# Performance work log

Hardware: AMD Instinct MI355X
Metric: run time of the kernel (lower is better)

## Reference

```python
import jax, jax.numpy as jnp
import numpy as np

N, D, R, L, E, EP = 50000, 256, 16, 2, 300000, 100000
SCALING = 16.0 / 16.0  # alpha / rank


def _ln(x, g, b, eps=1e-5):
    mu = x.mean(-1, keepdims=True)
    var = ((x - mu) ** 2).mean(-1, keepdims=True)
    return (x - mu) * jax.lax.rsqrt(var + eps) * g + b


def setup_inputs() -> dict:
    key = jax.random.key(0)
    ks = iter(jax.random.split(key, 32))
    f = lambda shp, s=0.05: jax.random.normal(next(ks), shp, jnp.float32) * s
    return dict(
        x=f((2, N, D), 1.0),
        W_in=f((2, D, D)), b_in=f((2, D)),
        lora_A=f((2, R, D)), lora_B=f((2, D, R), 0.01),
        pn_g=jnp.ones((2, D), jnp.float32), pn_b=jnp.zeros((2, D), jnp.float32),
        W_self=f((L, 2, D, D)), W_neigh=f((L, 2, D, D)), b_sage=f((L, 2, D)),
        ln_g=jnp.ones((L, 2, D), jnp.float32), ln_b=jnp.zeros((L, 2, D), jnp.float32),
        Wv=f((2, D, D)), bv=f((2, D)), Wo=f((2, D, D)), bo=f((2, D)),
        e_src=jax.random.randint(next(ks), (2, E), 0, N, jnp.int32),
        e_dst=jax.random.randint(next(ks), (2, E), 0, N, jnp.int32),
        pos_src=jax.random.randint(next(ks), (EP,), 0, N, jnp.int32),
        pos_dst=jax.random.randint(next(ks), (EP,), 0, N, jnp.int32),
        neg_src=jax.random.randint(next(ks), (EP,), 0, N, jnp.int32),
        neg_dst=jax.random.randint(next(ks), (EP,), 0, N, jnp.int32),
    )


def reference(x, W_in, b_in, lora_A, lora_B, pn_g, pn_b, W_self, W_neigh,
              b_sage, ln_g, ln_b, Wv, bv, Wo, bo,
              e_src, e_dst, pos_src, pos_dst, neg_src, neg_dst):
    # ---- per-type input projection + LoRA adapter + patient LayerNorm ----
    base = jnp.einsum('tnd,tod->tno', x, W_in) + b_in[:, None]
    ad = jnp.einsum('tnr,tdr->tnd', jnp.einsum('tnd,trd->tnr', x, lora_A), lora_B) * SCALING
    h = _ln(base + ad, pn_g[:, None], pn_b[:, None])  # [2, N, D]

    def seg_mean(v, i):  # mean aggregation over incoming edges
        s = jax.ops.segment_sum(v, i, num_segments=N)
        c = jax.ops.segment_sum(jnp.ones((i.shape[0], 1), v.dtype), i, num_segments=N)
        return s / jnp.maximum(c, 1.0)

    # ---- SAGE layers over blocks (relation 0: a->b, relation 1: b->a) ----
    for i in range(L):
        msgs = jax.vmap(lambda hr, sr: hr[sr])(h, e_src)      # [2, E, D], src type r
        agg = jax.vmap(seg_mean)(msgs, e_dst)                 # agg[r] lands at dst type 1-r
        neigh = agg[::-1]                                     # neigh[t] for node type t
        h_new = (jnp.einsum('tnd,tod->tno', h, W_self[i])
                 + jnp.einsum('tnd,tod->tno', neigh, W_neigh[i])
                 + b_sage[i][:, None])
        if i == L - 1:
            # nn.MultiheadAttention with seq_len=1: softmax over 1 key == 1,
            # so attn_out = out_proj(v_proj(x)).
            v = jnp.einsum('tnd,tod->tno', h_new, Wv) + bv[:, None]
            h_new = jnp.einsum('tnd,tod->tno', v, Wo) + bo[:, None]
        if i > 0:
            h_new = h_new + h  # residual (shapes always match)
        h = _ln(h_new, ln_g[i][:, None], ln_b[i][:, None])
        # dropout is identity at inference

    # ---- dot-product edge predictor on pos/neg graphs for etype (a, rel, b) ----
    h_a, h_b = h[0], h[1]
    pos_score = jnp.sum(h_a[pos_src] * h_b[pos_dst], axis=-1)
    neg_score = jnp.sum(h_a[neg_src] * h_b[neg_dst], axis=-1)
    return pos_score, neg_score
```

## Files before the change

### kernel.cpp

```cpp
#include <hip/hip_runtime.h>

#define D 256
#define BM 128
#define BN 128
#define BK 64
#define SCAN_NB 64
#define SCAN_T (SCAN_NB * 256)

typedef __attribute__((ext_vector_type(8))) short bf16x8;
typedef __attribute__((ext_vector_type(4))) float f32x4;
typedef __attribute__((ext_vector_type(4))) unsigned int u32x4;

union frag_cvt { u32x4 u; bf16x8 h; };

__device__ __forceinline__ unsigned short bf16_rn(float f) {
    const unsigned int u = __float_as_uint(f);
    return (unsigned short)((u + 0x7FFFu + ((u >> 16) & 1u)) >> 16);
}
__device__ __forceinline__ float bf16_to_f32(unsigned short s) {
    return __uint_as_float(((unsigned int)s) << 16);
}
__device__ __forceinline__ int xcd_logical(int bx, int NB) {
    const int q = NB >> 3, rem = NB & 7;
    const int xcd = bx & 7, slot = bx >> 3;
    return (xcd < rem) ? xcd * (q + 1) + slot
                       : rem * (q + 1) + (xcd - rem) * q + slot;
}

__global__ __launch_bounds__(256) void pre1_kernel(
    const float* __restrict__ W_in, const float* __restrict__ lA, const float* __restrict__ lB,
    unsigned short* __restrict__ win_eff,
    const float* __restrict__ W_self, unsigned short* __restrict__ ws0,
    const float* __restrict__ W_neigh, unsigned short* __restrict__ wn0,
    const float* __restrict__ Wo, const float* __restrict__ Wv, float* __restrict__ wvo,
    const float* __restrict__ bvp, const float* __restrict__ bo, float* __restrict__ bvo)
{
    const int b = blockIdx.x, tid = threadIdx.x;
    if (b < 512) {
        const int t = b >> 8, o = b & 255;
        float acc = W_in[((size_t)t * D + o) * D + tid];
        const float* Br = lB + ((size_t)t * D + o) * 16;
        const float* At = lA + (size_t)t * 16 * D;
        #pragma unroll
        for (int r = 0; r < 16; ++r) acc = fmaf(Br[r], At[r * D + tid], acc);
        win_eff[((size_t)t * D + o) * D + tid] = bf16_rn(acc);
    } else if (b < 1024) {
        const int i = (b - 512) * 256 + tid;
        ws0[i] = bf16_rn(W_self[i]);
    } else if (b < 1536) {
        const int i = (b - 1024) * 256 + tid;
        wn0[i] = bf16_rn(W_neigh[i]);
    } else if (b < 2048) {
        const int t = (b - 1536) >> 8, p = (b - 1536) & 255;
        const float* Xr = Wo + ((size_t)t * D + p) * D;
        const float* Yt = Wv + (size_t)t * D * D;
        float acc = 0.f;
        for (int o = 0; o < D; ++o) acc = fmaf(Xr[o], Yt[(size_t)o * D + tid], acc);
        wvo[((size_t)t * D + p) * D + tid] = acc;
    } else {
        const int t = b - 2048;
        const float* Mr = Wo + ((size_t)t * D + tid) * D;
        const float* vr = bvp + (size_t)t * D;
        float acc = bo[(size_t)t * D + tid];
        for (int o = 0; o < D; ++o) acc = fmaf(Mr[o], vr[o], acc);
        bvo[(size_t)t * D + tid] = acc;
    }
}

__global__ __launch_bounds__(256) void pre2_kernel(
    const float* __restrict__ wvo,
    const float* __restrict__ W_self1, unsigned short* __restrict__ ws1,
    const float* __restrict__ W_neigh1, unsigned short* __restrict__ wn1,
    const float* __restrict__ b_sage1, const float* __restrict__ bvo, float* __restrict__ b1e)
{
    const int b = blockIdx.x, tid = threadIdx.x;
    if (b < 512) {
        const int t = b >> 8, p = b & 255;
        const float* Xr = wvo + ((size_t)t * D + p) * D;
        const float* Yt = W_self1 + (size_t)t * D * D;
        float acc = 0.f;
        for (int o = 0; o < D; ++o) acc = fmaf(Xr[o], Yt[(size_t)o * D + tid], acc);
        ws1[((size_t)t * D + p) * D + tid] = bf16_rn(acc);
    } else if (b < 1024) {
        const int t = (b - 512) >> 8, p = (b - 512) & 255;
        const float* Xr = wvo + ((size_t)t * D + p) * D;
        const float* Yt = W_neigh1 + (size_t)t * D * D;
        float acc = 0.f;
        for (int o = 0; o < D; ++o) acc = fmaf(Xr[o], Yt[(size_t)o * D + tid], acc);
        wn1[((size_t)t * D + p) * D + tid] = bf16_rn(acc);
    } else {
        const int t = b - 1024;
        const float* Mr = wvo + ((size_t)t * D + tid) * D;
        const float* vr = b_sage1 + (size_t)t * D;
        float acc = bvo[(size_t)t * D + tid];
        for (int o = 0; o < D; ++o) acc = fmaf(Mr[o], vr[o], acc);
        b1e[(size_t)t * D + tid] = acc;
    }
}

__device__ __forceinline__ void load_bfrag(const unsigned short* __restrict__ Wp,
                                           int n0, int wn, int cidx, int rgrp,
                                           int kh, bf16x8 (&bq)[4][4])
{
    #pragma unroll
    for (int n = 0; n < 4; ++n) {
        const int o = n0 + wn + n * 16 + cidx;
        #pragma unroll
        for (int kk = 0; kk < 4; ++kk) {
            frag_cvt c;
            c.u = *(const u32x4*)(Wp + (size_t)o * D + kh * 128 + kk * 32 + rgrp * 8);
            bq[n][kk] = c.h;
        }
    }
}

__device__ __forceinline__ void gload_tile(const unsigned short* __restrict__ Abase,
                                           int r0, int kt, int tid, char* lbuf)
{
    const int wbase = (tid >> 6) << 10;
    #pragma unroll
    for (int c = 0; c < 4; ++c) {
        const int p   = c * 4096 + tid * 16;
        const int row = p >> 7;
        const int lwb = p & 127;
        const int lg  = lwb ^ ((row & 7) << 4);
        const unsigned short* g = Abase + (size_t)(r0 + row) * D + kt + (lg >> 1);
        char* l = lbuf + c * 4096 + wbase;
        __builtin_amdgcn_global_load_lds(
            (const __attribute__((address_space(1))) unsigned int*)g,
            (__attribute__((address_space(3))) unsigned int*)l, 16, 0, 0);
    }
}

__global__ __launch_bounds__(256, 2) void gemm_bf16_kernel(
    const unsigned short* __restrict__ A, const unsigned short* __restrict__ W1,
    const unsigned short* __restrict__ A2, const unsigned short* __restrict__ W2,
    const float* __restrict__ bias,
    unsigned short* __restrict__ Cbf, int M, int swap2)
{
    const int t   = blockIdx.z;
    const int logical = xcd_logical(blockIdx.x, gridDim.x);
    const int m0  = (logical >> 1) * BM;
    const int n0  = (logical & 1) * BN;
    const int tid = threadIdx.x;
    const int lane = tid & 63;
    const int wid  = tid >> 6;
    const int wm = (wid >> 1) * 64;
    const int wn = (wid & 1) * 64;
    const int rgrp = lane >> 4;
    const int cidx = lane & 15;

    __shared__ __align__(16) unsigned short SH[16384];
    char* AsB0 = (char*)SH;
    char* AsB1 = (char*)SH + 16384;

    const int t2 = swap2 ? (1 - t) : t;
    const unsigned short* Aps[2] = { A  + (size_t)t  * M * D, A2 + (size_t)t2 * M * D };
    const unsigned short* Wps[2] = { W1 + (size_t)t  * D * D, W2 + (size_t)t  * D * D };

    f32x4 acc[4][4];
    #pragma unroll
    for (int i = 0; i < 4; ++i)
        #pragma unroll
        for (int j = 0; j < 4; ++j)
            acc[i][j] = (f32x4){0.f, 0.f, 0.f, 0.f};

    bf16x8 bq[2][4][4];
    gload_tile(Aps[0], m0, 0, tid, AsB0);
    load_bfrag(Wps[0], n0, wn, cidx, rgrp, 0, bq[0]);

    #pragma unroll
    for (int idx = 0; idx < 8; ++idx) {
        __syncthreads();
        if (idx < 7)
            gload_tile(Aps[(idx + 1) >> 2], m0, ((idx + 1) & 3) * BK, tid,
                       (idx & 1) ? AsB0 : AsB1);
        if ((idx & 1) == 1 && idx < 7) {
            const int nh = (idx >> 1) + 1;
            load_bfrag(Wps[nh >> 1], n0, wn, cidx, rgrp, nh & 1, bq[nh & 1]);
        }
        const char* cb = (idx & 1) ? AsB1 : AsB0;
        const int half = idx >> 1;
        #pragma unroll
        for (int ks = 0; ks < 2; ++ks) {
            const int kb = ks * 64 + rgrp * 16;
            bf16x8 af[4];
            #pragma unroll
            for (int m = 0; m < 4; ++m) {
                const int row = wm + m * 16 + cidx;
                const int sw  = (row * 128 + kb) ^ ((row & 7) << 4);
                frag_cvt c; c.u = *(const u32x4*)(cb + sw); af[m] = c.h;
            }
            #pragma unroll
            for (int m = 0; m < 4; ++m)
                #pragma unroll
                for (int n = 0; n < 4; ++n)
                    acc[m][n] = __builtin_amdgcn_mfma_f32_16x16x32_bf16(
                        af[m], bq[half & 1][n][(idx & 1) * 2 + ks], acc[m][n], 0, 0, 0);
        }
        __syncthreads();
    }

    unsigned short* Ct = Cbf + (size_t)t * M * D;
    #pragma unroll
    for (int h = 0; h < 2; ++h) {
        __syncthreads();
        if ((wid >> 1) == h) {
            #pragma unroll
            for (int n = 0; n < 4; ++n) {
                const int col = wn + n * 16 + cidx;
                const float bc = bias[t * D + n0 + col];
                #pragma unroll
                for (int m = 0; m < 4; ++m) {
                    const int rw = (wm & 63) + m * 16 + rgrp * 4;
                    #pragma unroll
                    for (int i = 0; i < 4; ++i)
                        SH[(rw + i) * 136 + col] = bf16_rn(acc[m][n][i] + bc);
                }
            }
        }
        __syncthreads();
        #pragma unroll
        for (int it = 0; it < 2; ++it) {
            const int g   = tid + it * 256;
            const int row = g >> 3;
            const int cg  = g & 7;
            const int grow = m0 + h * 64 + row;
            if (grow < M) {
                const u32x4 lo = *(const u32x4*)&SH[row * 136 + cg * 16];
                const u32x4 hi = *(const u32x4*)&SH[row * 136 + cg * 16 + 8];
                u32x4* dst = (u32x4*)(Ct + (size_t)grow * D + n0 + cg * 16);
                dst[0] = lo;
                dst[1] = hi;
            }
        }
    }
}

__global__ __launch_bounds__(128, 2) void gemm_in_kernel(
    const float* __restrict__ X, const unsigned short* __restrict__ Wb,
    const float* __restrict__ bias, unsigned short* __restrict__ Cbf, int M)
{
    const int t   = blockIdx.z;
    const int logical = xcd_logical(blockIdx.x, gridDim.x);
    const int m0  = (logical >> 1) * 64;
    const int n0  = (logical & 1) * BN;
    const int tid = threadIdx.x;
    const int lane = tid & 63;
    const int wid  = tid >> 6;
    const int wn = wid * 64;
    const int rgrp = lane >> 4;
    const int cidx = lane & 15;

    __shared__ __align__(16) unsigned short SH[8704];
    char* AsB = (char*)SH;

    const float* Xp = X + (size_t)t * M * D;
    const unsigned short* Wp = Wb + (size_t)t * D * D;

    f32x4 acc[4][4];
    #pragma unroll
    for (int i = 0; i < 4; ++i)
        #pragma unroll
        for (int j = 0; j < 4; ++j)
            acc[i][j] = (f32x4){0.f, 0.f, 0.f, 0.f};

    bf16x8 bq[2][4][4];
    float4 xr0[4], xr1[4];
    #pragma unroll
    for (int it = 0; it < 4; ++it) {
        const int g = tid + it * 128;
        const int row = g >> 3;
        const int kg = g & 7;
        const int ar = min(m0 + row, M - 1);
        xr0[it] = *(const float4*)(Xp + (size_t)ar * D + kg * 8);
        xr1[it] = *(const float4*)(Xp + (size_t)ar * D + kg * 8 + 4);
    }
    load_bfrag(Wp, n0, wn, cidx, rgrp, 0, bq[0]);

    #pragma unroll
    for (int kt_i = 0; kt_i < 4; ++kt_i) {
        #pragma unroll
        for (int it = 0; it < 4; ++it) {
            const int g = tid + it * 128;
            const int row = g >> 3;
            const int kg = g & 7;
            unsigned int w[4];
            w[0] = ((unsigned int)bf16_rn(xr0[it].y) << 16) | bf16_rn(xr0[it].x);
            w[1] = ((unsigned int)bf16_rn(xr0[it].w) << 16) | bf16_rn(xr0[it].z);
            w[2] = ((unsigned int)bf16_rn(xr1[it].y) << 16) | bf16_rn(xr1[it].x);
            w[3] = ((unsigned int)bf16_rn(xr1[it].w) << 16) | bf16_rn(xr1[it].z);
            const int sw = ((row * BK + kg * 8) * 2) ^ ((row & 7) << 4);
            *(u32x4*)(AsB + sw) = (u32x4){w[0], w[1], w[2], w[3]};
        }
        __syncthreads();
        if (kt_i < 3) {
            const int kt = (kt_i + 1) * BK;
            #pragma unroll
            for (int it = 0; it < 4; ++it) {
                const int g = tid + it * 128;
                const int row = g >> 3;
                const int kg = g & 7;
                const int ar = min(m0 + row, M - 1);
                xr0[it] = *(const float4*)(Xp + (size_t)ar * D + kt + kg * 8);
                xr1[it] = *(const float4*)(Xp + (size_t)ar * D + kt + kg * 8 + 4);
            }
        }
        if (kt_i == 1) load_bfrag(Wp, n0, wn, cidx, rgrp, 1, bq[1]);
        #pragma unroll
        for (int ks = 0; ks < 2; ++ks) {
            const int kb = ks * 64 + rgrp * 16;
            bf16x8 af[4];
            #pragma unroll
            for (int m = 0; m < 4; ++m) {
                const int row = m * 16 + cidx;
                const int sw  = (row * 128 + kb) ^ ((row & 7) << 4);
                frag_cvt c; c.u = *(u32x4*)(AsB + sw); af[m] = c.h;
            }
            #pragma unroll
            for (int m = 0; m < 4; ++m)
                #pragma unroll
                for (int n = 0; n < 4; ++n)
                    acc[m][n] = __builtin_amdgcn_mfma_f32_16x16x32_bf16(
                        af[m], bq[kt_i >> 1][n][(kt_i & 1) * 2 + ks], acc[m][n], 0, 0, 0);
        }
        __syncthreads();
    }

    #pragma unroll
    for (int n = 0; n < 4; ++n) {
        const int col = wn + n * 16 + cidx;
        const float bc = bias[t * D + n0 + col];
        #pragma unroll
        for (int m = 0; m < 4; ++m) {
            const int rowb = m * 16 + rgrp * 4;
            #pragma unroll
            for (int i = 0; i < 4; ++i)
                SH[(rowb + i) * 136 + col] = bf16_rn(acc[m][n][i] + bc);
        }
    }
    __syncthreads();
    unsigned short* Ct = Cbf + (size_t)t * M * D;
    #pragma unroll
    for (int it = 0; it < 4; ++it) {
        const int g   = tid + it * 128;
        const int row = g >> 3;
        const int cg  = g & 7;
        const int grow = m0 + row;
        if (grow < M) {
            const u32x4 lo = *(const u32x4*)&SH[row * 136 + cg * 16];
            const u32x4 hi = *(const u32x4*)&SH[row * 136 + cg * 16 + 8];
            u32x4* dst = (u32x4*)(Ct + (size_t)grow * D + n0 + cg * 16);
            dst[0] = lo;
            dst[1] = hi;
        }
    }
}

__global__ __launch_bounds__(256) void ln_wave_kernel(
    const unsigned short* __restrict__ in_bf, const unsigned short* __restrict__ res_bf,
    const float* __restrict__ g, const float* __restrict__ b,
    unsigned short* __restrict__ out_bf, int N)
{
    const int row  = (blockIdx.x * 256 + threadIdx.x) >> 6;
    const int lane = threadIdx.x & 63;
    if (row >= 2 * N) return;
    const int t = (row >= N) ? 1 : 0;
    const ushort4 iv = *(const ushort4*)(in_bf + (size_t)row * D + lane * 4);
    float4 v = make_float4(bf16_to_f32(iv.x), bf16_to_f32(iv.y),
                           bf16_to_f32(iv.z), bf16_to_f32(iv.w));
    if (res_bf) {
        const ushort4 rv = *(const ushort4*)(res_bf + (size_t)row * D + lane * 4);
        v.x += bf16_to_f32(rv.x); v.y += bf16_to_f32(rv.y);
        v.z += bf16_to_f32(rv.z); v.w += bf16_to_f32(rv.w);
    }
    float s = v.x + v.y + v.z + v.w;
    #pragma unroll
    for (int off = 32; off > 0; off >>= 1) s += __shfl_xor(s, off);
    const float mu = s * (1.0f / 256.0f);
    const float4 dl = make_float4(v.x - mu, v.y - mu, v.z - mu, v.w - mu);
    float q = dl.x * dl.x + dl.y * dl.y + dl.z * dl.z + dl.w * dl.w;
    #pragma unroll
    for (int off = 32; off > 0; off >>= 1) q += __shfl_xor(q, off);
    const float rstd = rsqrtf(q * (1.0f / 256.0f) + 1e-5f);
    const float4 gv = *(const float4*)(g + (size_t)t * D + lane * 4);
    const float4 bv = *(const float4*)(b + (size_t)t * D + lane * 4);
    ushort4 ob;
    ob.x = bf16_rn(dl.x * rstd * gv.x + bv.x);
    ob.y = bf16_rn(dl.y * rstd * gv.y + bv.y);
    ob.z = bf16_rn(dl.z * rstd * gv.z + bv.z);
    ob.w = bf16_rn(dl.w * rstd * gv.w + bv.w);
    *(ushort4*)(out_bf + (size_t)row * D + lane * 4) = ob;
}

__global__ void count_kernel(const int* __restrict__ e_dst, int* __restrict__ cnt,
                             int E2, int N, int E)
{
    const int i = blockIdx.x * 256 + threadIdx.x;
    if (i >= E2) return;
    const int t = i / E;
    atomicAdd(&cnt[(size_t)t * N + e_dst[i]], 1);
}

__global__ __launch_bounds__(256) void scan1_kernel(const int* __restrict__ cnt,
                                                    int* __restrict__ texcl,
                                                    int* __restrict__ bsum, int n, int c)
{
    __shared__ int ts[256];
    const int tid = threadIdx.x;
    const int gt  = blockIdx.x * 256 + tid;
    const int b   = gt * c;
    const int e   = min(b + c, n);
    int s = 0;
    for (int i = b; i < e; ++i) s += cnt[i];
    ts[tid] = s;
    __syncthreads();
    #pragma unroll
    for (int off = 1; off < 256; off <<= 1) {
        const int v = (tid >= off) ? ts[tid - off] : 0;
        __syncthreads();
        ts[tid] += v;
        __syncthreads();
    }
    texcl[gt] = ts[tid] - s;
    if (tid == 255) bsum[blockIdx.x] = ts[255];
}

__global__ __launch_bounds__(64) void scan2_kernel(int* __restrict__ bsum,
                                                   int* __restrict__ bbase,
                                                   int* __restrict__ offs, int n, int nb)
{
    const int lane = threadIdx.x;
    int v = (lane < nb) ? bsum[lane] : 0;
    int s = v;
    #pragma unroll
    for (int off = 1; off < 64; off <<= 1) {
        const int u = __shfl_up(s, off);
        if (lane >= off) s += u;
    }
    if (lane < nb) bbase[lane] = s - v;
    if (lane == 63) offs[n] = s;
}

__global__ __launch_bounds__(256) void scan3_kernel(const int* __restrict__ cnt,
                                                    const int* __restrict__ texcl,
                                                    const int* __restrict__ bbase,
                                                    int* __restrict__ offs, int n, int c)
{
    const int tid = threadIdx.x;
    const int gt  = blockIdx.x * 256 + tid;
    const int b   = gt * c;
    const int e   = min(b + c, n);
    int base = bbase[blockIdx.x] + texcl[gt];
    for (int i = b; i < e; ++i) { offs[i] = base; base += cnt[i]; }
}

__global__ void fill_kernel(const int* __restrict__ e_src, const int* __restrict__ e_dst,
                            const int* __restrict__ offs, int* __restrict__ cur,
                            int* __restrict__ sorted, int E2, int N, int E)
{
    const int i = blockIdx.x * 256 + threadIdx.x;
    if (i >= E2) return;
    const int t = i / E;
    const int idx = t * N + e_dst[i];
    const int pos = offs[idx] + atomicAdd(&cur[idx], 1);
    sorted[pos] = e_src[i];
}

__global__ __launch_bounds__(256) void agg_kernel(
    const unsigned short* __restrict__ hbf, const int* __restrict__ sorted_src,
    const int* __restrict__ offs, unsigned short* __restrict__ aggbf, int N)
{
    const int gw   = (blockIdx.x * 256 + threadIdx.x) >> 6;
    const int lane = threadIdx.x & 63;
    if (gw >= 2 * N) return;
    const int t = (gw >= N) ? 1 : 0;
    const int beg = offs[gw];
    const int end = offs[gw + 1];
    const unsigned short* hb = hbf + (size_t)t * N * D;
    float4 a0 = make_float4(0.f, 0.f, 0.f, 0.f);
    float4 a1 = make_float4(0.f, 0.f, 0.f, 0.f);
    int e = beg;
    for (; e + 2 <= end; e += 2) {
        const int s0 = sorted_src[e];
        const int s1 = sorted_src[e + 1];
        const ushort4 v0 = *(const ushort4*)(hb + (size_t)s0 * D + lane * 4);
        const ushort4 v1 = *(const ushort4*)(hb + (size_t)s1 * D + lane * 4);
        a0.x += bf16_to_f32(v0.x); a0.y += bf16_to_f32(v0.y);
        a0.z += bf16_to_f32(v0.z); a0.w += bf16_to_f32(v0.w);
        a1.x += bf16_to_f32(v1.x); a1.y += bf16_to_f32(v1.y);
        a1.z += bf16_to_f32(v1.z); a1.w += bf16_to_f32(v1.w);
    }
    if (e < end) {
        const int s0 = sorted_src[e];
        const ushort4 v0 = *(const ushort4*)(hb + (size_t)s0 * D + lane * 4);
        a0.x += bf16_to_f32(v0.x); a0.y += bf16_to_f32(v0.y);
        a0.z += bf16_to_f32(v0.z); a0.w += bf16_to_f32(v0.w);
    }
    const float inv = 1.0f / fmaxf((float)(end - beg), 1.0f);
    ushort4 o;
    o.x = bf16_rn((a0.x + a1.x) * inv); o.y = bf16_rn((a0.y + a1.y) * inv);
    o.z = bf16_rn((a0.z + a1.z) * inv); o.w = bf16_rn((a0.w + a1.w) * inv);
    *(ushort4*)(aggbf + (size_t)gw * D + lane * 4) = o;
}

__global__ __launch_bounds__(256) void score_kernel(
    const unsigned short* __restrict__ h,
    const int* __restrict__ pos_src, const int* __restrict__ pos_dst,
    const int* __restrict__ neg_src, const int* __restrict__ neg_dst,
    float* __restrict__ out, int EP, int N)
{
    const int wid  = (blockIdx.x * 256 + threadIdx.x) >> 6;
    const int lane = threadIdx.x & 63;
    if (wid >= 2 * EP) return;
    const int kind = wid / EP;
    const int k    = wid - kind * EP;
    const int s = kind ? neg_src[k] : pos_src[k];
    const int d = kind ? neg_dst[k] : pos_dst[k];
    const ushort4 a = *(const ushort4*)(h + (size_t)s * D + lane * 4);
    const ushort4 b = *(const ushort4*)(h + ((size_t)N + d) * D + lane * 4);
    float v = bf16_to_f32(a.x) * bf16_to_f32(b.x)
            + bf16_to_f32(a.y) * bf16_to_f32(b.y)
            + bf16_to_f32(a.z) * bf16_to_f32(b.z)
            + bf16_to_f32(a.w) * bf16_to_f32(b.w);
    #pragma unroll
    for (int off = 32; off > 0; off >>= 1) v += __shfl_down(v, off);
    if (lane == 0) out[wid] = v;
}

extern "C" void kernel_launch(void* const* d_in, const int* in_sizes, int n_in,
                              void* d_out, int out_size, void* d_ws, size_t ws_size,
                              hipStream_t stream)
{
    const float* x      = (const float*)d_in[0];
    const float* W_in   = (const float*)d_in[1];
    const float* b_in   = (const float*)d_in[2];
    const float* lora_A = (const float*)d_in[3];
    const float* lora_B = (const float*)d_in[4];
    const float* pn_g   = (const float*)d_in[5];
    const float* pn_b   = (const float*)d_in[6];
    const float* W_self = (const float*)d_in[7];
    const float* W_neigh= (const float*)d_in[8];
    const float* b_sage = (const float*)d_in[9];
    const float* ln_g   = (const float*)d_in[10];
    const float* ln_b   = (const float*)d_in[11];
    const float* Wv     = (const float*)d_in[12];
    const float* bvp    = (const float*)d_in[13];
    const float* Wo     = (const float*)d_in[14];
    const float* bo     = (const float*)d_in[15];
    const int* e_src    = (const int*)d_in[16];
    const int* e_dst    = (const int*)d_in[17];
    const int* pos_src  = (const int*)d_in[18];
    const int* pos_dst  = (const int*)d_in[19];
    const int* neg_src  = (const int*)d_in[20];
    const int* neg_dst  = (const int*)d_in[21];

    const int N  = in_sizes[0] / (2 * D);
    const int E  = in_sizes[16] / 2;
    const int EP = in_sizes[18];
    const size_t ND2 = (size_t)2 * N * D;
    const size_t DD2 = (size_t)2 * D * D;
    const int n2 = 2 * N;

    unsigned short* P0 = (unsigned short*)d_ws;
    unsigned short* P1 = P0 + ND2;
    unsigned short* P2 = P1 + ND2;
    unsigned short* T  = P2 + ND2;
    int* cnt    = (int*)(T + ND2);
    int* cur    = cnt + (size_t)n2;
    int* offs   = cur + (size_t)n2;
    int* sorted = offs + (size_t)n2 + 1;
    int* texcl  = sorted + (size_t)2 * E;
    int* bsum   = texcl + SCAN_T;
    int* bbase  = bsum + SCAN_NB;
    float* wvo  = (float*)(bbase + SCAN_NB);
    float* bvo  = wvo + DD2;
    float* b1e  = bvo + 2 * D;
    unsigned short* win_eff = (unsigned short*)(b1e + 2 * D);
    unsigned short* ws0 = win_eff + DD2;
    unsigned short* wn0 = ws0 + DD2;
    unsigned short* ws1 = wn0 + DD2;
    unsigned short* wn1 = ws1 + DD2;

    pre1_kernel<<<2050, 256, 0, stream>>>(W_in, lora_A, lora_B, win_eff,
                                          W_self, ws0, W_neigh, wn0,
                                          Wo, Wv, wvo, bvp, bo, bvo);
    pre2_kernel<<<1026, 256, 0, stream>>>(wvo, W_self + DD2, ws1,
                                          W_neigh + DD2, wn1,
                                          b_sage + 2 * D, bvo, b1e);

    hipMemsetAsync(cnt, 0, (size_t)2 * n2 * sizeof(int), stream);
    count_kernel<<<(2 * E + 255) / 256, 256, 0, stream>>>(e_dst, cnt, 2 * E, N, E);
    const int sc = (n2 + SCAN_T - 1) / SCAN_T;
    scan1_kernel<<<SCAN_NB, 256, 0, stream>>>(cnt, texcl, bsum, n2, sc);
    scan2_kernel<<<1, 64, 0, stream>>>(bsum, bbase, offs, n2, SCAN_NB);
    scan3_kernel<<<SCAN_NB, 256, 0, stream>>>(cnt, texcl, bbase, offs, n2, sc);
    fill_kernel<<<(2 * E + 255) / 256, 256, 0, stream>>>(e_src, e_dst, offs, cur, sorted, 2 * E, N, E);

    const dim3 gblk128(128);
    const dim3 gblk(256);
    const int mpan_l = (N + BM - 1) / BM;
    const int mpan_i = (N + 63) / 64;
    const dim3 ggrid(2 * mpan_l, 1, 2);
    const dim3 ggrid_in(2 * mpan_i, 1, 2);
    const int ln_grid = (2 * N + 3) / 4;

    gemm_in_kernel<<<ggrid_in, gblk128, 0, stream>>>(x, win_eff, b_in, T, N);
    ln_wave_kernel<<<ln_grid, gblk, 0, stream>>>(T, nullptr, pn_g, pn_b, P0, N);

    agg_kernel<<<dim3((2 * N + 3) / 4, 1, 1), gblk, 0, stream>>>(P0, sorted, offs, P1, N);
    gemm_bf16_kernel<<<ggrid, gblk, 0, stream>>>(P0, ws0, P1, wn0, b_sage, T, N, 1);
    ln_wave_kernel<<<ln_grid, gblk, 0, stream>>>(T, nullptr, ln_g, ln_b, P2, N);

    agg_kernel<<<dim3((2 * N + 3) / 4, 1, 1), gblk, 0, stream>>>(P2, sorted, offs, P1, N);
    gemm_bf16_kernel<<<ggrid, gblk, 0, stream>>>(P2, ws1, P1, wn1, b1e, T, N, 1);
    ln_wave_kernel<<<ln_grid, gblk, 0, stream>>>(T, P2, ln_g + 2 * D, ln_b + 2 * D, P0, N);

    score_kernel<<<(2 * EP + 3) / 4, gblk, 0, stream>>>(P0, pos_src, pos_dst, neg_src, neg_dst,
                                                        (float*)d_out, EP, N);
}
```

Measured before the change: 529.7 us.

## Fuse LayerNorm into GEMM epilogues with full-width 64-row tiles

The GEMM kernels are retiled so that each block computes a full 256-wide output row panel of 64 rows, with four waves each covering 64 columns. This lets bias, residual add and LayerNorm be done in the epilogue through a cross-wave shared-memory reduction, so the separate ln_wave kernels and the intermediate bf16 round trip through T disappear. The cost is smaller M tiles with the whole N width per block, extra barriers in the epilogue, and no XCD-aware block remapping.

```diff
diff --git a/kernel.cpp b/kernel.cpp
--- a/kernel.cpp
+++ b/kernel.cpp
@@ -1,8 +1,6 @@
 #include <hip/hip_runtime.h>
 
 #define D 256
-#define BM 128
-#define BN 128
 #define BK 64
 #define SCAN_NB 64
 #define SCAN_T (SCAN_NB * 256)
@@ -19,12 +17,6 @@
 }
 __device__ __forceinline__ float bf16_to_f32(unsigned short s) {
     return __uint_as_float(((unsigned int)s) << 16);
-}
-__device__ __forceinline__ int xcd_logical(int bx, int NB) {
-    const int q = NB >> 3, rem = NB & 7;
-    const int xcd = bx & 7, slot = bx >> 3;
-    return (xcd < rem) ? xcd * (q + 1) + slot
-                       : rem * (q + 1) + (xcd - rem) * q + slot;
 }
 
 __global__ __launch_bounds__(256) void pre1_kernel(
@@ -99,12 +91,12 @@
 }
 
 __device__ __forceinline__ void load_bfrag(const unsigned short* __restrict__ Wp,
-                                           int n0, int wn, int cidx, int rgrp,
+                                           int wn, int cidx, int rgrp,
                                            int kh, bf16x8 (&bq)[4][4])
 {
     #pragma unroll
     for (int n = 0; n < 4; ++n) {
-        const int o = n0 + wn + n * 16 + cidx;
+        const int o = wn + n * 16 + cidx;
         #pragma unroll
         for (int kk = 0; kk < 4; ++kk) {
             frag_cvt c;
@@ -114,12 +106,12 @@
     }
 }
 
-__device__ __forceinline__ void gload_tile(const unsigned short* __restrict__ Abase,
-                                           int r0, int kt, int tid, char* lbuf)
+__device__ __forceinline__ void gload_tile64(const unsigned short* __restrict__ Abase,
+                                             int r0, int kt, int tid, char* lbuf)
 {
     const int wbase = (tid >> 6) << 10;
     #pragma unroll
-    for (int c = 0; c < 4; ++c) {
+    for (int c = 0; c < 2; ++c) {
         const int p   = c * 4096 + tid * 16;
         const int row = p >> 7;
         const int lwb = p & 127;
@@ -132,119 +124,114 @@
     }
 }
 
-__global__ __launch_bounds__(256, 2) void gemm_bf16_kernel(
+__device__ __forceinline__ void ln_epilogue(
+    f32x4 (&acc)[4][4], unsigned short* SH,
+    const float* __restrict__ bias, const unsigned short* __restrict__ res_bf,
+    const float* __restrict__ g, const float* __restrict__ b,
+    unsigned short* __restrict__ out_bf,
+    int t, int m0, int M, int tid, int wid, int rgrp, int cidx, int wn)
+{
+    #pragma unroll
+    for (int n = 0; n < 4; ++n) {
+        const float bc = bias[t * D + wn + n * 16 + cidx];
+        #pragma unroll
+        for (int m = 0; m < 4; ++m)
+            #pragma unroll
+            for (int i = 0; i < 4; ++i)
+                acc[m][n][i] += bc;
+    }
+    if (res_bf) {
+        #pragma unroll
+        for (int m = 0; m < 4; ++m)
+            #pragma unroll
+            for (int i = 0; i < 4; ++i) {
+                const int row = m * 16 + rgrp * 4 + i;
+                const int gr  = min(m0 + row, M - 1);
+                const unsigned short* rr = res_bf + ((size_t)t * M + gr) * D + wn + cidx;
+                #pragma unroll
+                for (int n = 0; n < 4; ++n)
+                    acc[m][n][i] += bf16_to_f32(rr[n * 16]);
+            }
+    }
+    float* red  = (float*)((char*)SH + 16384);
+    float* red2 = red + 256;
+    float mu[4][4], rs[4][4];
+    #pragma unroll
+    for (int m = 0; m < 4; ++m)
+        #pragma unroll
+        for (int i = 0; i < 4; ++i) {
+            float s = 0.f;
+            #pragma unroll
+            for (int n = 0; n < 4; ++n) s += acc[m][n][i];
+            s += __shfl_xor(s, 1); s += __shfl_xor(s, 2);
+            s += __shfl_xor(s, 4); s += __shfl_xor(s, 8);
+            if (cidx == 0) red[(m * 16 + rgrp * 4 + i) * 4 + wid] = s;
+        }
+    __syncthreads();
+    #pragma unroll
+    for (int m = 0; m < 4; ++m)
+        #pragma unroll
+        for (int i = 0; i < 4; ++i) {
+            const int row = m * 16 + rgrp * 4 + i;
+            mu[m][i] = (red[row * 4] + red[row * 4 + 1] +
+                        red[row * 4 + 2] + red[row * 4 + 3]) * (1.0f / 256.0f);
+            float q = 0.f;
+            #pragma unroll
+            for (int n = 0; n < 4; ++n) {
+                const float d0 = acc[m][n][i] - mu[m][i];
+                q += d0 * d0;
+            }
+            q += __shfl_xor(q, 1); q += __shfl_xor(q, 2);
+            q += __shfl_xor(q, 4); q += __shfl_xor(q, 8);
+            if (cidx == 0) red2[row * 4 + wid] = q;
+        }
+    __syncthreads();
+    #pragma unroll
+    for (int m = 0; m < 4; ++m)
+        #pragma unroll
+        for (int i = 0; i < 4; ++i) {
+            const int row = m * 16 + rgrp * 4 + i;
+            rs[m][i] = rsqrtf((red2[row * 4] + red2[row * 4 + 1] +
+                               red2[row * 4 + 2] + red2[row * 4 + 3]) * (1.0f / 256.0f) + 1e-5f);
+        }
+    __syncthreads();
+    #pragma unroll
+    for (int n = 0; n < 4; ++n) {
+        const int col = wn + n * 16 + cidx;
+        const float gv = g[t * D + col];
+        const float bv = b[t * D + col];
+        #pragma unroll
+        for (int m = 0; m < 4; ++m)
+            #pragma unroll
+            for (int i = 0; i < 4; ++i) {
+                const int row = m * 16 + rgrp * 4 + i;
+                SH[row * 264 + col] = bf16_rn((acc[m][n][i] - mu[m][i]) * rs[m][i] * gv + bv);
+            }
+    }
+    __syncthreads();
+    unsigned short* Ct = out_bf + (size_t)t * M * D;
+    #pragma unroll
+    for (int it = 0; it < 8; ++it) {
+        const int gidx = tid + it * 256;
+        const int row  = gidx >> 5;
+        const int cg   = gidx & 31;
+        const int grow = m0 + row;
+        if (grow < M) {
+            const u32x4 v = *(const u32x4*)&SH[row * 264 + cg * 8];
+            *(u32x4*)(Ct + (size_t)grow * D + cg * 8) = v;
+        }
+    }
+}
+
+__global__ __launch_bounds__(256, 2) void gemm_ln_kernel(
     const unsigned short* __restrict__ A, const unsigned short* __restrict__ W1,
     const unsigned short* __restrict__ A2, const unsigned short* __restrict__ W2,
-    const float* __restrict__ bias,
-    unsigned short* __restrict__ Cbf, int M, int swap2)
+    const float* __restrict__ bias, const unsigned short* __restrict__ res_bf,
+    const float* __restrict__ g, const float* __restrict__ b,
+    unsigned short* __restrict__ out_bf, int M, int swap2)
 {
     const int t   = blockIdx.z;
-    const int logical = xcd_logical(blockIdx.x, gridDim.x);
-    const int m0  = (logical >> 1) * BM;
-    const int n0  = (logical & 1) * BN;
-    const int tid = threadIdx.x;
-    const int lane = tid & 63;
-    const int wid  = tid >> 6;
-    const int wm = (wid >> 1) * 64;
-    const int wn = (wid & 1) * 64;
-    const int rgrp = lane >> 4;
-    const int cidx = lane & 15;
-
-    __shared__ __align__(16) unsigned short SH[16384];
-    char* AsB0 = (char*)SH;
-    char* AsB1 = (char*)SH + 16384;
-
-    const int t2 = swap2 ? (1 - t) : t;
-    const unsigned short* Aps[2] = { A  + (size_t)t  * M * D, A2 + (size_t)t2 * M * D };
-    const unsigned short* Wps[2] = { W1 + (size_t)t  * D * D, W2 + (size_t)t  * D * D };
-
-    f32x4 acc[4][4];
-    #pragma unroll
-    for (int i = 0; i < 4; ++i)
-        #pragma unroll
-        for (int j = 0; j < 4; ++j)
-            acc[i][j] = (f32x4){0.f, 0.f, 0.f, 0.f};
-
-    bf16x8 bq[2][4][4];
-    gload_tile(Aps[0], m0, 0, tid, AsB0);
-    load_bfrag(Wps[0], n0, wn, cidx, rgrp, 0, bq[0]);
-
-    #pragma unroll
-    for (int idx = 0; idx < 8; ++idx) {
-        __syncthreads();
-        if (idx < 7)
-            gload_tile(Aps[(idx + 1) >> 2], m0, ((idx + 1) & 3) * BK, tid,
-                       (idx & 1) ? AsB0 : AsB1);
-        if ((idx & 1) == 1 && idx < 7) {
-            const int nh = (idx >> 1) + 1;
-            load_bfrag(Wps[nh >> 1], n0, wn, cidx, rgrp, nh & 1, bq[nh & 1]);
-        }
-        const char* cb = (idx & 1) ? AsB1 : AsB0;
-        const int half = idx >> 1;
-        #pragma unroll
-        for (int ks = 0; ks < 2; ++ks) {
-            const int kb = ks * 64 + rgrp * 16;
-            bf16x8 af[4];
-            #pragma unroll
-            for (int m = 0; m < 4; ++m) {
-                const int row = wm + m * 16 + cidx;
-                const int sw  = (row * 128 + kb) ^ ((row & 7) << 4);
-                frag_cvt c; c.u = *(const u32x4*)(cb + sw); af[m] = c.h;
-            }
-            #pragma unroll
-            for (int m = 0; m < 4; ++m)
-                #pragma unroll
-                for (int n = 0; n < 4; ++n)
-                    acc[m][n] = __builtin_amdgcn_mfma_f32_16x16x32_bf16(
-                        af[m], bq[half & 1][n][(idx & 1) * 2 + ks], acc[m][n], 0, 0, 0);
-        }
-        __syncthreads();
-    }
-
-    unsigned short* Ct = Cbf + (size_t)t * M * D;
-    #pragma unroll
-    for (int h = 0; h < 2; ++h) {
-        __syncthreads();
-        if ((wid >> 1) == h) {
-            #pragma unroll
-            for (int n = 0; n < 4; ++n) {
-                const int col = wn + n * 16 + cidx;
-                const float bc = bias[t * D + n0 + col];
-                #pragma unroll
-                for (int m = 0; m < 4; ++m) {
-                    const int rw = (wm & 63) + m * 16 + rgrp * 4;
-                    #pragma unroll
-                    for (int i = 0; i < 4; ++i)
-                        SH[(rw + i) * 136 + col] = bf16_rn(acc[m][n][i] + bc);
-                }
-            }
-        }
-        __syncthreads();
-        #pragma unroll
-        for (int it = 0; it < 2; ++it) {
-            const int g   = tid + it * 256;
-            const int row = g >> 3;
-            const int cg  = g & 7;
-            const int grow = m0 + h * 64 + row;
-            if (grow < M) {
-                const u32x4 lo = *(const u32x4*)&SH[row * 136 + cg * 16];
-                const u32x4 hi = *(const u32x4*)&SH[row * 136 + cg * 16 + 8];
-                u32x4* dst = (u32x4*)(Ct + (size_t)grow * D + n0 + cg * 16);
-                dst[0] = lo;
-                dst[1] = hi;
-            }
-        }
-    }
-}
-
-__global__ __launch_bounds__(128, 2) void gemm_in_kernel(
-    const float* __restrict__ X, const unsigned short* __restrict__ Wb,
-    const float* __restrict__ bias, unsigned short* __restrict__ Cbf, int M)
-{
-    const int t   = blockIdx.z;
-    const int logical = xcd_logical(blockIdx.x, gridDim.x);
-    const int m0  = (logical >> 1) * 64;
-    const int n0  = (logical & 1) * BN;
+    const int m0  = blockIdx.x * 64;
     const int tid = threadIdx.x;
     const int lane = tid & 63;
     const int wid  = tid >> 6;
@@ -252,7 +239,76 @@
     const int rgrp = lane >> 4;
     const int cidx = lane & 15;
 
-    __shared__ __align__(16) unsigned short SH[8704];
+    __shared__ __align__(16) unsigned short SH[64 * 264];
+    char* AsB0 = (char*)SH;
+    char* AsB1 = (char*)SH + 8192;
+
+    const int t2 = swap2 ? (1 - t) : t;
+    const unsigned short* Aps[2] = { A  + (size_t)t  * M * D, A2 + (size_t)t2 * M * D };
+    const unsigned short* Wps[2] = { W1 + (size_t)t  * D * D, W2 + (size_t)t  * D * D };
+
+    f32x4 acc[4][4];
+    #pragma unroll
+    for (int i = 0; i < 4; ++i)
+        #pragma unroll
+        for (int j = 0; j < 4; ++j)
+            acc[i][j] = (f32x4){0.f, 0.f, 0.f, 0.f};
+
+    bf16x8 bq[2][4][4];
+    gload_tile64(Aps[0], m0, 0, tid, AsB0);
+    load_bfrag(Wps[0], wn, cidx, rgrp, 0, bq[0]);
+
+    #pragma unroll
+    for (int idx = 0; idx < 8; ++idx) {
+        __syncthreads();
+        if (idx < 7)
+            gload_tile64(Aps[(idx + 1) >> 2], m0, ((idx + 1) & 3) * BK, tid,
+                         (idx & 1) ? AsB0 : AsB1);
+        if ((idx & 1) == 1 && idx < 7) {
+            const int nh = (idx >> 1) + 1;
+            load_bfrag(Wps[nh >> 1], wn, cidx, rgrp, nh & 1, bq[nh & 1]);
+        }
+        const char* cb = (idx & 1) ? AsB1 : AsB0;
+        const int half = idx >> 1;
+        #pragma unroll
+        for (int ks = 0; ks < 2; ++ks) {
+            const int kb = ks * 64 + rgrp * 16;
+            bf16x8 af[4];
+            #pragma unroll
+            for (int m = 0; m < 4; ++m) {
+                const int row = m * 16 + cidx;
+                const int sw  = (row * 128 + kb) ^ ((row & 7) << 4);
+                frag_cvt c; c.u = *(const u32x4*)(cb + sw); af[m] = c.h;
+            }
+            #pragma unroll
+            for (int m = 0; m < 4; ++m)
+                #pragma unroll
+                for (int n = 0; n < 4; ++n)
+                    acc[m][n] = __builtin_amdgcn_mfma_f32_16x16x32_bf16(
+                        af[m], bq[half & 1][n][(idx & 1) * 2 + ks], acc[m][n], 0, 0, 0);
+        }
+        __syncthreads();
+    }
+
+    ln_epilogue(acc, SH, bias, res_bf, g, b, out_bf, t, m0, M, tid, wid, rgrp, cidx, wn);
+}
+
+__global__ __launch_bounds__(256, 2) void gemm_ln_in_kernel(
+    const float* __restrict__ X, const unsigned short* __restrict__ Wb,
+    const float* __restrict__ bias,
+    const float* __restrict__ g, const float* __restrict__ b,
+    unsigned short* __restrict__ out_bf, int M)
+{
+    const int t   = blockIdx.z;
+    const int m0  = blockIdx.x * 64;
+    const int tid = threadIdx.x;
+    const int lane = tid & 63;
+    const int wid  = tid >> 6;
+    const int wn = wid * 64;
+    const int rgrp = lane >> 4;
+    const int cidx = lane & 15;
+
+    __shared__ __align__(16) unsigned short SH[64 * 264];
     char* AsB = (char*)SH;
 
     const float* Xp = X + (size_t)t * M * D;
@@ -266,25 +322,25 @@
             acc[i][j] = (f32x4){0.f, 0.f, 0.f, 0.f};
 
     bf16x8 bq[2][4][4];
-    float4 xr0[4], xr1[4];
-    #pragma unroll
-    for (int it = 0; it < 4; ++it) {
-        const int g = tid + it * 128;
-        const int row = g >> 3;
-        const int kg = g & 7;
+    float4 xr0[2], xr1[2];
+    #pragma unroll
+    for (int it = 0; it < 2; ++it) {
+        const int gi = tid + it * 256;
+        const int row = gi >> 3;
+        const int kg = gi & 7;
         const int ar = min(m0 + row, M - 1);
         xr0[it] = *(const float4*)(Xp + (size_t)ar * D + kg * 8);
         xr1[it] = *(const float4*)(Xp + (size_t)ar * D + kg * 8 + 4);
     }
-    load_bfrag(Wp, n0, wn, cidx, rgrp, 0, bq[0]);
+    load_bfrag(Wp, wn, cidx, rgrp, 0, bq[0]);
 
     #pragma unroll
     for (int kt_i = 0; kt_i < 4; ++kt_i) {
         #pragma unroll
-        for (int it = 0; it < 4; ++it) {
-            const int g = tid + it * 128;
-            const int row = g >> 3;
-            const int kg = g & 7;
+        for (int it = 0; it < 2; ++it) {
+            const int gi = tid + it * 256;
+            const int row = gi >> 3;
+            const int kg = gi & 7;
             unsigned int w[4];
             w[0] = ((unsigned int)bf16_rn(xr0[it].y) << 16) | bf16_rn(xr0[it].x);
             w[1] = ((unsigned int)bf16_rn(xr0[it].w) << 16) | bf16_rn(xr0[it].z);
@@ -297,16 +353,16 @@
         if (kt_i < 3) {
             const int kt = (kt_i + 1) * BK;
             #pragma unroll
-            for (int it = 0; it < 4; ++it) {
-                const int g = tid + it * 128;
-                const int row = g >> 3;
-                const int kg = g & 7;
+            for (int it = 0; it < 2; ++it) {
+                const int gi = tid + it * 256;
+                const int row = gi >> 3;
+                const int kg = gi & 7;
                 const int ar = min(m0 + row, M - 1);
                 xr0[it] = *(const float4*)(Xp + (size_t)ar * D + kt + kg * 8);
                 xr1[it] = *(const float4*)(Xp + (size_t)ar * D + kt + kg * 8 + 4);
             }
         }
-        if (kt_i == 1) load_bfrag(Wp, n0, wn, cidx, rgrp, 1, bq[1]);
+        if (kt_i == 1) load_bfrag(Wp, wn, cidx, rgrp, 1, bq[1]);
         #pragma unroll
         for (int ks = 0; ks < 2; ++ks) {
             const int kb = ks * 64 + rgrp * 16;
@@ -327,70 +383,7 @@
         __syncthreads();
     }
 
-    #pragma unroll
-    for (int n = 0; n < 4; ++n) {
-        const int col = wn + n * 16 + cidx;
-        const float bc = bias[t * D + n0 + col];
-        #pragma unroll
-        for (int m = 0; m < 4; ++m) {
-            const int rowb = m * 16 + rgrp * 4;
-            #pragma unroll
-            for (int i = 0; i < 4; ++i)
-                SH[(rowb + i) * 136 + col] = bf16_rn(acc[m][n][i] + bc);
-        }
-    }
-    __syncthreads();
-    unsigned short* Ct = Cbf + (size_t)t * M * D;
-    #pragma unroll
-    for (int it = 0; it < 4; ++it) {
-        const int g   = tid + it * 128;
-        const int row = g >> 3;
-        const int cg  = g & 7;
-        const int grow = m0 + row;
-        if (grow < M) {
-            const u32x4 lo = *(const u32x4*)&SH[row * 136 + cg * 16];
-            const u32x4 hi = *(const u32x4*)&SH[row * 136 + cg * 16 + 8];
-            u32x4* dst = (u32x4*)(Ct + (size_t)grow * D + n0 + cg * 16);
-            dst[0] = lo;
-            dst[1] = hi;
-        }
-    }
-}
-
-__global__ __launch_bounds__(256) void ln_wave_kernel(
-    const unsigned short* __restrict__ in_bf, const unsigned short* __restrict__ res_bf,
-    const float* __restrict__ g, const float* __restrict__ b,
-    unsigned short* __restrict__ out_bf, int N)
-{
-    const int row  = (blockIdx.x * 256 + threadIdx.x) >> 6;
-    const int lane = threadIdx.x & 63;
-    if (row >= 2 * N) return;
-    const int t = (row >= N) ? 1 : 0;
-    const ushort4 iv = *(const ushort4*)(in_bf + (size_t)row * D + lane * 4);
-    float4 v = make_float4(bf16_to_f32(iv.x), bf16_to_f32(iv.y),
-                           bf16_to_f32(iv.z), bf16_to_f32(iv.w));
-    if (res_bf) {
-        const ushort4 rv = *(const ushort4*)(res_bf + (size_t)row * D + lane * 4);
-        v.x += bf16_to_f32(rv.x); v.y += bf16_to_f32(rv.y);
-        v.z += bf16_to_f32(rv.z); v.w += bf16_to_f32(rv.w);
-    }
-    float s = v.x + v.y + v.z + v.w;
-    #pragma unroll
-    for (int off = 32; off > 0; off >>= 1) s += __shfl_xor(s, off);
-    const float mu = s * (1.0f / 256.0f);
-    const float4 dl = make_float4(v.x - mu, v.y - mu, v.z - mu, v.w - mu);
-    float q = dl.x * dl.x + dl.y * dl.y + dl.z * dl.z + dl.w * dl.w;
-    #pragma unroll
-    for (int off = 32; off > 0; off >>= 1) q += __shfl_xor(q, off);
-    const float rstd = rsqrtf(q * (1.0f / 256.0f) + 1e-5f);
-    const float4 gv = *(const float4*)(g + (size_t)t * D + lane * 4);
-    const float4 bv = *(const float4*)(b + (size_t)t * D + lane * 4);
-    ushort4 ob;
-    ob.x = bf16_rn(dl.x * rstd * gv.x + bv.x);
-    ob.y = bf16_rn(dl.y * rstd * gv.y + bv.y);
-    ob.z = bf16_rn(dl.z * rstd * gv.z + bv.z);
-    ob.w = bf16_rn(dl.w * rstd * gv.w + bv.w);
-    *(ushort4*)(out_bf + (size_t)row * D + lane * 4) = ob;
+    ln_epilogue(acc, SH, bias, nullptr, g, b, out_bf, t, m0, M, tid, wid, rgrp, cidx, wn);
 }
 
 __global__ void count_kernel(const int* __restrict__ e_dst, int* __restrict__ cnt,
@@ -597,24 +590,19 @@
     scan3_kernel<<<SCAN_NB, 256, 0, stream>>>(cnt, texcl, bbase, offs, n2, sc);
     fill_kernel<<<(2 * E + 255) / 256, 256, 0, stream>>>(e_src, e_dst, offs, cur, sorted, 2 * E, N, E);
 
-    const dim3 gblk128(128);
     const dim3 gblk(256);
-    const int mpan_l = (N + BM - 1) / BM;
-    const int mpan_i = (N + 63) / 64;
-    const dim3 ggrid(2 * mpan_l, 1, 2);
-    const dim3 ggrid_in(2 * mpan_i, 1, 2);
-    const int ln_grid = (2 * N + 3) / 4;
-
-    gemm_in_kernel<<<ggrid_in, gblk128, 0, stream>>>(x, win_eff, b_in, T, N);
-    ln_wave_kernel<<<ln_grid, gblk, 0, stream>>>(T, nullptr, pn_g, pn_b, P0, N);
+    const int mpan = (N + 63) / 64;
+    const dim3 fgrid(mpan, 1, 2);
+
+    gemm_ln_in_kernel<<<fgrid, gblk, 0, stream>>>(x, win_eff, b_in, pn_g, pn_b, P0, N);
 
     agg_kernel<<<dim3((2 * N + 3) / 4, 1, 1), gblk, 0, stream>>>(P0, sorted, offs, P1, N);
-    gemm_bf16_kernel<<<ggrid, gblk, 0, stream>>>(P0, ws0, P1, wn0, b_sage, T, N, 1);
-    ln_wave_kernel<<<ln_grid, gblk, 0, stream>>>(T, nullptr, ln_g, ln_b, P2, N);
+    gemm_ln_kernel<<<fgrid, gblk, 0, stream>>>(P0, ws0, P1, wn0, b_sage, nullptr,
+                                               ln_g, ln_b, P2, N, 1);
 
     agg_kernel<<<dim3((2 * N + 3) / 4, 1, 1), gblk, 0, stream>>>(P2, sorted, offs, P1, N);
-    gemm_bf16_kernel<<<ggrid, gblk, 0, stream>>>(P2, ws1, P1, wn1, b1e, T, N, 1);
-    ln_wave_kernel<<<ln_grid, gblk, 0, stream>>>(T, P2, ln_g + 2 * D, ln_b + 2 * D, P0, N);
+    gemm_ln_kernel<<<fgrid, gblk, 0, stream>>>(P2, ws1, P1, wn1, b1e, P2,
+                                               ln_g + 2 * D, ln_b + 2 * D, P0, N, 1);
 
     score_kernel<<<(2 * EP + 3) / 4, gblk, 0, stream>>>(P0, pos_src, pos_dst, neg_src, neg_dst,
                                                         (float*)d_out, EP, N);
```

Measured after the change: 466.5 us. -11.9%, faster.
